# Optimization experiments

Hardware: AMD Instinct MI355X
Metric: run time of the kernel (lower is better)

Reference implementation:

```python
import jax, jax.numpy as jnp
import numpy as np

B, P, N, C = 8, 4, 512, 768
H = 12
HD = C // H  # 64
SCALE = HD ** -0.5


def setup_inputs() -> dict:
    key = jax.random.key(0)
    k1, k2, k3 = jax.random.split(key, 3)
    x = jax.random.normal(k1, (B, P, N, C), dtype=jnp.float32)
    W_qkv = jax.random.normal(k2, (3 * C, C), dtype=jnp.float32) * (C ** -0.5)
    W_proj = jax.random.normal(k3, (C, C), dtype=jnp.float32) * (C ** -0.5)
    b_proj = jnp.zeros((C,), dtype=jnp.float32)
    return {"x": x, "W_qkv": W_qkv, "W_proj": W_proj, "b_proj": b_proj}


def reference(x, W_qkv, W_proj, b_proj):
    b, p, n, c = x.shape
    # qkv projection (no bias): (B,P,N,3C) -> (B,P,N,3,H,HD)
    qkv = jnp.einsum('bpnc,dc->bpnd', x, W_qkv).reshape(b, p, n, 3, H, HD)
    # -> (3, B, P, H, N, HD)
    qkv = jnp.transpose(qkv, (3, 0, 1, 4, 2, 5))
    q, k, v = qkv[0], qkv[1], qkv[2]
    # scaled dot-product attention per (batch, patch, head)
    attn = jnp.einsum('bphnd,bphmd->bphnm', q * SCALE, k)
    attn = jax.nn.softmax(attn, axis=-1)
    out = jnp.einsum('bphnm,bphmd->bphnd', attn, v)
    # merge heads: (B,P,N,H,HD) -> (B,P,N,C)
    out = jnp.transpose(out, (0, 1, 3, 2, 4)).reshape(b, p, n, c)
    return jnp.einsum('bpnc,dc->bpnd', out, W_proj) + b_proj
```

## Files before the change

### kernel.cpp

```cpp
#include <hip/hip_runtime.h>

typedef _Float16 f16x8 __attribute__((ext_vector_type(8)));
typedef _Float16 f16x4 __attribute__((ext_vector_type(4)));
typedef unsigned short u16x8 __attribute__((ext_vector_type(8)));
typedef unsigned short u16x4 __attribute__((ext_vector_type(4)));
typedef float f32x4 __attribute__((ext_vector_type(4)));

#define GLOAD_LDS16(GP, LP)                                                        \
  __builtin_amdgcn_global_load_lds((const __attribute__((address_space(1))) void*)(GP), \
                                   (__attribute__((address_space(3))) void*)(LP), 16, 0, 0)

__device__ __forceinline__ unsigned int pkh(float a, float b) {
  return __builtin_bit_cast(unsigned int, __builtin_amdgcn_cvt_pkrtz(a, b));
}
__device__ __forceinline__ f16x8 ldfragh(const unsigned short* p) {
  return __builtin_bit_cast(f16x8, *(const u16x8*)p);
}
__device__ __forceinline__ f16x4 ldfragh4(const unsigned short* p) {
  return __builtin_bit_cast(f16x4, *(const u16x4*)p);
}
__device__ __forceinline__ f32x4 mfma32h(f16x8 a, f16x8 b, f32x4 c) {
  return __builtin_amdgcn_mfma_f32_16x16x32_f16(a, b, c, 0, 0, 0);
}
__device__ __forceinline__ f32x4 mfma16h(f16x4 a, f16x4 b, f32x4 c) {
  return __builtin_amdgcn_mfma_f32_16x16x16f16(a, b, c, 0, 0, 0);
}

#define MTOK   16384
#define CDIM   768
#define C3     2304
#define C2     1536
#define NX     12582912
#define NQW    1769472
#define NPW    589824

#define QSCALE_LOG2E 0.1803368801111204f

#define XB_OFF    0ul
#define WQKV_OFF  25165824ul
#define WPROJ_OFF 28704768ul
#define QK_OFF    29884416ul
#define VT_OFF    80216064ul

__global__ __launch_bounds__(256) void convert_kernel(
    const float* __restrict__ x, const float* __restrict__ wqkv,
    const float* __restrict__ wproj, unsigned short* __restrict__ xb,
    unsigned short* __restrict__ wqkvb, unsigned short* __restrict__ wprojb) {
  const int NX4 = NX / 4, NQ4 = NQW / 4, NP4 = NPW / 4;
  const int total = NX4 + NQ4 + NP4;
  for (int i = blockIdx.x * 256 + threadIdx.x; i < total; i += gridDim.x * 256) {
    const float4* src; unsigned short* dst; float scale = 1.f; int j;
    if (i < NX4) { src = (const float4*)x; dst = xb; j = i; }
    else if (i < NX4 + NQ4) {
      j = i - NX4; src = (const float4*)wqkv; dst = wqkvb;
      int d = (j * 4) / CDIM; if (d < CDIM) scale = QSCALE_LOG2E;
    } else { j = i - NX4 - NQ4; src = (const float4*)wproj; dst = wprojb; }
    float4 v = src[j];
    uint2 pk; pk.x = pkh(v.x * scale, v.y * scale); pk.y = pkh(v.z * scale, v.w * scale);
    *(uint2*)(dst + (long)j * 4) = pk;
  }
}

template <int MODE>
__global__ __launch_bounds__(256) void gemm_bt(
    const unsigned short* __restrict__ A, const unsigned short* __restrict__ B,
    unsigned short* __restrict__ out_hf, float* __restrict__ out_f32,
    const float* __restrict__ bias) {
  constexpr int K = 768;
  constexpr int NT = K / 64;
  constexpr bool SWAP = (MODE != 1);
  __shared__ unsigned short As[2][128 * 64];
  __shared__ unsigned short Bs[2][128 * 64];
  const int tid = threadIdx.x;
  const int wave = tid >> 6, lane = tid & 63;
  const int wy = wave >> 1, wx = wave & 1;
  const int l15 = lane & 15, quad = lane >> 4;
  const int bm = blockIdx.x, bn = blockIdx.y;

  f32x4 acc[4][4];
  for (int i = 0; i < 4; i++)
    for (int j = 0; j < 4; j++) acc[i][j] = f32x4{0.f, 0.f, 0.f, 0.f};

  const unsigned short* Ab = A + (long)bm * 128 * K;
  const unsigned short* Bb = B + (long)bn * 128 * K;

  long goff[4]; int ldsoff[4];
  for (int i = 0; i < 4; i++) {
    int c = wave * 256 + i * 64 + lane;
    int row = c >> 3, q = c & 7;
    int srcq = q ^ (row & 7);
    goff[i] = (long)row * K + srcq * 8;
    ldsoff[i] = c * 8;
  }
  const int slot0 = (quad ^ (l15 & 7)) * 8;
  const int slot1 = ((4 + quad) ^ (l15 & 7)) * 8;

  for (int i = 0; i < 4; i++) {
    GLOAD_LDS16(Ab + goff[i], &As[0][ldsoff[i]]);
    GLOAD_LDS16(Bb + goff[i], &Bs[0][ldsoff[i]]);
  }

  for (int t = 0; t < NT; t++) {
    __syncthreads();
    if (t + 1 < NT) {
      const long kk = (long)(t + 1) * 64;
      const int nb = (t + 1) & 1;
      for (int i = 0; i < 4; i++) {
        GLOAD_LDS16(Ab + goff[i] + kk, &As[nb][ldsoff[i]]);
        GLOAD_LDS16(Bb + goff[i] + kk, &Bs[nb][ldsoff[i]]);
      }
    }
    const unsigned short* Ac = As[t & 1];
    const unsigned short* Bc = Bs[t & 1];
    for (int ks = 0; ks < 2; ks++) {
      const int sl = ks ? slot1 : slot0;
      f16x8 af[4], bfr[4];
      for (int mt = 0; mt < 4; mt++) af[mt]  = ldfragh(Ac + (wy * 64 + mt * 16 + l15) * 64 + sl);
      for (int nt = 0; nt < 4; nt++) bfr[nt] = ldfragh(Bc + (wx * 64 + nt * 16 + l15) * 64 + sl);
      for (int mt = 0; mt < 4; mt++)
        for (int nt = 0; nt < 4; nt++) {
          if (SWAP) acc[mt][nt] = mfma32h(bfr[nt], af[mt], acc[mt][nt]);
          else      acc[mt][nt] = mfma32h(af[mt], bfr[nt], acc[mt][nt]);
        }
    }
  }

  if (MODE == 0) {
    for (int mt = 0; mt < 4; mt++) {
      int m = bm * 128 + wy * 64 + mt * 16 + l15;
      for (int nt = 0; nt < 4; nt++) {
        int d0 = bn * 128 + wx * 64 + nt * 16 + quad * 4;
        uint2 pk; pk.x = pkh(acc[mt][nt][0], acc[mt][nt][1]);
        pk.y = pkh(acc[mt][nt][2], acc[mt][nt][3]);
        *(uint2*)(out_hf + (long)m * C2 + d0) = pk;
      }
    }
  } else if (MODE == 1) {
    for (int mt = 0; mt < 4; mt++) {
      int mg = bm * 128 + wy * 64 + mt * 16 + quad * 4;
      int bp = mg >> 9, n0 = mg & 511;
      for (int nt = 0; nt < 4; nt++) {
        int dp = bn * 128 + wx * 64 + nt * 16 + l15;
        int hh = dp >> 6, e = dp & 63;
        uint2 pk; pk.x = pkh(acc[mt][nt][0], acc[mt][nt][1]);
        pk.y = pkh(acc[mt][nt][2], acc[mt][nt][3]);
        *(uint2*)(out_hf + ((long)((bp * 12 + hh) * 64 + e) * 512 + n0)) = pk;
      }
    }
  } else {
    for (int nt = 0; nt < 4; nt++) {
      int d0 = bn * 128 + wx * 64 + nt * 16 + quad * 4;
      float4 bv = *(const float4*)(bias + d0);
      for (int mt = 0; mt < 4; mt++) {
        int m = bm * 128 + wy * 64 + mt * 16 + l15;
        float4 o;
        o.x = acc[mt][nt][0] + bv.x; o.y = acc[mt][nt][1] + bv.y;
        o.z = acc[mt][nt][2] + bv.z; o.w = acc[mt][nt][3] + bv.w;
        *(float4*)(out_f32 + (long)m * CDIM + d0) = o;
      }
    }
  }
}

__global__ __launch_bounds__(256, 4) void attn_kernel(
    const unsigned short* __restrict__ qk, const unsigned short* __restrict__ vT,
    unsigned short* __restrict__ aout) {
  const int bph = blockIdx.x;
  const int qt  = blockIdx.y;
  const int bp = bph / 12, h = bph % 12;
  const int tid = threadIdx.x;
  const int wave = tid >> 6, lane = tid & 63;
  const int l15 = lane & 15, quad = lane >> 4;

  __shared__ unsigned short Qs[128 * 72];
  __shared__ unsigned short Ks[64 * 72];
  __shared__ unsigned short Vs[64 * 72];

  const unsigned short* Qg = qk + (long)(bp * 512 + qt * 128) * C2 + h * 64;
  const unsigned short* Kg = qk + (long)(bp * 512) * C2 + CDIM + h * 64;
  const unsigned short* Vg = vT + (long)(bp * 12 + h) * 64 * 512;

  for (int i = 0; i < 4; i++) {
    int c = tid + i * 256;
    int row = c >> 3, c8 = c & 7;
    *(uint4*)(Qs + row * 72 + c8 * 8) = *(const uint4*)(Qg + (long)row * C2 + c8 * 8);
  }

  f32x4 o[2][4];
  float lrow[2] = {0.f, 0.f};
  for (int a = 0; a < 2; a++)
    for (int b = 0; b < 4; b++) o[a][b] = f32x4{0.f, 0.f, 0.f, 0.f};

  for (int ch = 0; ch < 8; ch++) {
    if (ch) __syncthreads();
    for (int i = 0; i < 2; i++) {
      int c = tid + i * 256;
      int row = c >> 3, c8 = c & 7;
      *(uint4*)(Ks + row * 72 + c8 * 8) = *(const uint4*)(Kg + (long)(ch * 64 + row) * C2 + c8 * 8);
      *(uint4*)(Vs + row * 72 + c8 * 8) = *(const uint4*)(Vg + (long)row * 512 + ch * 64 + c8 * 8);
    }
    __syncthreads();

    f32x4 st[2][4];
    for (int a = 0; a < 2; a++)
      for (int b = 0; b < 4; b++) st[a][b] = f32x4{0.f, 0.f, 0.f, 0.f};
    for (int ks = 0; ks < 2; ks++) {
      f16x8 qf[2];
      qf[0] = ldfragh(Qs + (wave * 32 +      l15) * 72 + ks * 32 + quad * 8);
      qf[1] = ldfragh(Qs + (wave * 32 + 16 + l15) * 72 + ks * 32 + quad * 8);
      for (int nt = 0; nt < 4; nt++) {
        f16x8 kf = ldfragh(Ks + (nt * 16 + l15) * 72 + ks * 32 + quad * 8);
        st[0][nt] = mfma32h(kf, qf[0], st[0][nt]);
        st[1][nt] = mfma32h(kf, qf[1], st[1][nt]);
      }
    }

    f16x4 pf[2][4];
    for (int mt2 = 0; mt2 < 2; mt2++) {
      float rs = 0.f;
      for (int nt = 0; nt < 4; nt++) {
        f32x4 p;
        for (int r = 0; r < 4; r++) {
          p[r] = __builtin_amdgcn_exp2f(st[mt2][nt][r]);
          rs += p[r];
        }
        uint2 pk2; pk2.x = pkh(p[0], p[1]); pk2.y = pkh(p[2], p[3]);
        pf[mt2][nt] = __builtin_bit_cast(f16x4, pk2);
      }
      lrow[mt2] += rs;
    }

    for (int nt = 0; nt < 4; nt++)
      for (int et = 0; et < 4; et++) {
        f16x4 vf = ldfragh4(Vs + (et * 16 + l15) * 72 + nt * 16 + quad * 4);
        o[0][et] = mfma16h(vf, pf[0][nt], o[0][et]);
        o[1][et] = mfma16h(vf, pf[1][nt], o[1][et]);
      }
  }

  for (int mt2 = 0; mt2 < 2; mt2++) {
    float l = lrow[mt2];
    l += __shfl_xor(l, 16);
    l += __shfl_xor(l, 32);
    float inv = 1.f / l;
    int q = qt * 128 + wave * 32 + mt2 * 16 + l15;
    for (int et = 0; et < 4; et++) {
      uint2 pk; pk.x = pkh(o[mt2][et][0] * inv, o[mt2][et][1] * inv);
      pk.y = pkh(o[mt2][et][2] * inv, o[mt2][et][3] * inv);
      *(uint2*)(aout + (long)(bp * 512 + q) * CDIM + h * 64 + et * 16 + quad * 4) = pk;
    }
  }
}

extern "C" void kernel_launch(void* const* d_in, const int* in_sizes, int n_in,
                              void* d_out, int out_size, void* d_ws, size_t ws_size,
                              hipStream_t stream) {
  (void)in_sizes; (void)n_in; (void)out_size; (void)ws_size;
  const float* x     = (const float*)d_in[0];
  const float* wqkv  = (const float*)d_in[1];
  const float* wproj = (const float*)d_in[2];
  const float* bproj = (const float*)d_in[3];
  float* out = (float*)d_out;
  char* ws = (char*)d_ws;

  unsigned short* xb     = (unsigned short*)(ws + XB_OFF);
  unsigned short* wqkvb  = (unsigned short*)(ws + WQKV_OFF);
  unsigned short* wprojb = (unsigned short*)(ws + WPROJ_OFF);
  unsigned short* qkbuf  = (unsigned short*)(ws + QK_OFF);
  unsigned short* vTbuf  = (unsigned short*)(ws + VT_OFF);
  unsigned short* attn_o = xb;

  convert_kernel<<<2048, 256, 0, stream>>>(x, wqkv, wproj, xb, wqkvb, wprojb);
  gemm_bt<0><<<dim3(128, 12), 256, 0, stream>>>(xb, wqkvb, qkbuf, nullptr, nullptr);
  gemm_bt<1><<<dim3(128, 6), 256, 0, stream>>>(xb, wqkvb + (long)C2 * CDIM, vTbuf, nullptr, nullptr);
  attn_kernel<<<dim3(384, 4), 256, 0, stream>>>(qkbuf, vTbuf, attn_o);
  gemm_bt<2><<<dim3(128, 6), 256, 0, stream>>>(attn_o, wprojb, nullptr, out, bproj);
}
```

Baseline: 267.9 us.

## Fuse QK and V projection GEMMs into one launch with grouped block order

Result: faster. 260.4 us (-2.8%).

```diff
diff --git a/kernel.cpp b/kernel.cpp
--- a/kernel.cpp
+++ b/kernel.cpp
@@ -61,21 +61,25 @@
   }
 }
 
-template <int MODE>
+template <int MODE, int NCOLS>
 __global__ __launch_bounds__(256) void gemm_bt(
     const unsigned short* __restrict__ A, const unsigned short* __restrict__ B,
-    unsigned short* __restrict__ out_hf, float* __restrict__ out_f32,
-    const float* __restrict__ bias) {
+    unsigned short* __restrict__ out_hf, unsigned short* __restrict__ out_vT,
+    float* __restrict__ out_f32, const float* __restrict__ bias) {
   constexpr int K = 768;
   constexpr int NT = K / 64;
-  constexpr bool SWAP = (MODE != 1);
   __shared__ unsigned short As[2][128 * 64];
   __shared__ unsigned short Bs[2][128 * 64];
   const int tid = threadIdx.x;
   const int wave = tid >> 6, lane = tid & 63;
   const int wy = wave >> 1, wx = wave & 1;
   const int l15 = lane & 15, quad = lane >> 4;
-  const int bm = blockIdx.x, bn = blockIdx.y;
+
+  const int gid = blockIdx.x;
+  const int g = gid >> 3;
+  const int bm = ((g / NCOLS) << 3) + (gid & 7);
+  const int bn = g % NCOLS;
+  const bool swap = (MODE == 2) || (bn < 12);
 
   f32x4 acc[4][4];
   for (int i = 0; i < 4; i++)
@@ -117,34 +121,40 @@
       f16x8 af[4], bfr[4];
       for (int mt = 0; mt < 4; mt++) af[mt]  = ldfragh(Ac + (wy * 64 + mt * 16 + l15) * 64 + sl);
       for (int nt = 0; nt < 4; nt++) bfr[nt] = ldfragh(Bc + (wx * 64 + nt * 16 + l15) * 64 + sl);
-      for (int mt = 0; mt < 4; mt++)
+      if (swap) {
+        for (int mt = 0; mt < 4; mt++)
+          for (int nt = 0; nt < 4; nt++)
+            acc[mt][nt] = mfma32h(bfr[nt], af[mt], acc[mt][nt]);
+      } else {
+        for (int mt = 0; mt < 4; mt++)
+          for (int nt = 0; nt < 4; nt++)
+            acc[mt][nt] = mfma32h(af[mt], bfr[nt], acc[mt][nt]);
+      }
+    }
+  }
+
+  if (MODE == 0) {
+    if (bn < 12) {
+      for (int mt = 0; mt < 4; mt++) {
+        int m = bm * 128 + wy * 64 + mt * 16 + l15;
         for (int nt = 0; nt < 4; nt++) {
-          if (SWAP) acc[mt][nt] = mfma32h(bfr[nt], af[mt], acc[mt][nt]);
-          else      acc[mt][nt] = mfma32h(af[mt], bfr[nt], acc[mt][nt]);
+          int d0 = bn * 128 + wx * 64 + nt * 16 + quad * 4;
+          uint2 pk; pk.x = pkh(acc[mt][nt][0], acc[mt][nt][1]);
+          pk.y = pkh(acc[mt][nt][2], acc[mt][nt][3]);
+          *(uint2*)(out_hf + (long)m * C2 + d0) = pk;
         }
-    }
-  }
-
-  if (MODE == 0) {
-    for (int mt = 0; mt < 4; mt++) {
-      int m = bm * 128 + wy * 64 + mt * 16 + l15;
-      for (int nt = 0; nt < 4; nt++) {
-        int d0 = bn * 128 + wx * 64 + nt * 16 + quad * 4;
-        uint2 pk; pk.x = pkh(acc[mt][nt][0], acc[mt][nt][1]);
-        pk.y = pkh(acc[mt][nt][2], acc[mt][nt][3]);
-        *(uint2*)(out_hf + (long)m * C2 + d0) = pk;
-      }
-    }
-  } else if (MODE == 1) {
-    for (int mt = 0; mt < 4; mt++) {
-      int mg = bm * 128 + wy * 64 + mt * 16 + quad * 4;
-      int bp = mg >> 9, n0 = mg & 511;
-      for (int nt = 0; nt < 4; nt++) {
-        int dp = bn * 128 + wx * 64 + nt * 16 + l15;
-        int hh = dp >> 6, e = dp & 63;
-        uint2 pk; pk.x = pkh(acc[mt][nt][0], acc[mt][nt][1]);
-        pk.y = pkh(acc[mt][nt][2], acc[mt][nt][3]);
-        *(uint2*)(out_hf + ((long)((bp * 12 + hh) * 64 + e) * 512 + n0)) = pk;
+      }
+    } else {
+      for (int mt = 0; mt < 4; mt++) {
+        int mg = bm * 128 + wy * 64 + mt * 16 + quad * 4;
+        int bp = mg >> 9, n0 = mg & 511;
+        for (int nt = 0; nt < 4; nt++) {
+          int dp = bn * 128 - C2 + wx * 64 + nt * 16 + l15;
+          int hh = dp >> 6, e = dp & 63;
+          uint2 pk; pk.x = pkh(acc[mt][nt][0], acc[mt][nt][1]);
+          pk.y = pkh(acc[mt][nt][2], acc[mt][nt][3]);
+          *(uint2*)(out_vT + ((long)((bp * 12 + hh) * 64 + e) * 512 + n0)) = pk;
+        }
       }
     }
   } else {
@@ -271,8 +281,7 @@
   unsigned short* attn_o = xb;
 
   convert_kernel<<<2048, 256, 0, stream>>>(x, wqkv, wproj, xb, wqkvb, wprojb);
-  gemm_bt<0><<<dim3(128, 12), 256, 0, stream>>>(xb, wqkvb, qkbuf, nullptr, nullptr);
-  gemm_bt<1><<<dim3(128, 6), 256, 0, stream>>>(xb, wqkvb + (long)C2 * CDIM, vTbuf, nullptr, nullptr);
+  gemm_bt<0, 18><<<128 * 18, 256, 0, stream>>>(xb, wqkvb, qkbuf, vTbuf, nullptr, nullptr);
   attn_kernel<<<dim3(384, 4), 256, 0, stream>>>(qkbuf, vTbuf, attn_o);
-  gemm_bt<2><<<dim3(128, 6), 256, 0, stream>>>(attn_o, wprojb, nullptr, out, bproj);
-}
+  gemm_bt<2, 6><<<128 * 6, 256, 0, stream>>>(attn_o, wprojb, nullptr, nullptr, out, bproj);
+}
```
